# Performance work log

Measured on AMD Instinct MI355X. Metric: run time of the kernel, lower is better.

Reference implementation:

```python
import jax, jax.numpy as jnp
import numpy as np

HEAD = 16
CONV = 32
DEF = CONV * 8  # 256
SCALE = jnp.float32(np.sqrt(DEF))  # sqrt(256) = 16


def setup_inputs() -> dict:
    key = jax.random.key(0)
    k1, k2, k3, k4 = jax.random.split(key, 4)
    bsz = 4096
    drug = jax.random.normal(k1, (bsz, DEF), dtype=jnp.float32)
    protein = jax.random.normal(k2, (bsz, DEF), dtype=jnp.float32)
    # Linear(256 -> 4096) weights, stored [in, out]; bias zeros
    W_d = jax.random.normal(k3, (DEF, DEF * HEAD), dtype=jnp.float32) * (1.0 / np.sqrt(DEF))
    b_d = jnp.zeros((DEF * HEAD,), dtype=jnp.float32)
    W_p = jax.random.normal(k4, (DEF, DEF * HEAD), dtype=jnp.float32) * (1.0 / np.sqrt(DEF))
    b_p = jnp.zeros((DEF * HEAD,), dtype=jnp.float32)
    return {"drug": drug, "protein": protein, "W_d": W_d, "b_d": b_d, "W_p": W_p, "b_p": b_p}


def reference(drug, protein, W_d, b_d, W_p, b_p):
    bsz = drug.shape[0]
    # ReLU(linear) then reshape: drug -> [b, 256, head]; protein -> [b, head, 256]
    drug_att = jax.nn.relu(drug @ W_d + b_d).reshape(bsz, DEF, HEAD)
    protein_att = jax.nn.relu(protein @ W_p + b_p).reshape(bsz, HEAD, DEF)
    # interaction map [b, 256, 256]
    imap = jnp.tanh(jnp.einsum('bdh,bhp->bdp', drug_att, protein_att) / SCALE)
    compound_atte = jnp.tanh(jnp.sum(imap, axis=2))  # [b, 256]
    protein_atte = jnp.tanh(jnp.sum(imap, axis=1))   # [b, 256]
    return (drug * compound_atte, protein * protein_atte)
```

## Files before the change

kernel.cpp:

```cpp
#include <hip/hip_runtime.h>
#include <stdint.h>

typedef unsigned short u16;
typedef u16   u16x4 __attribute__((ext_vector_type(4)));
typedef u16   u16x8 __attribute__((ext_vector_type(8)));
typedef short v8s   __attribute__((ext_vector_type(8)));
typedef float v4f   __attribute__((ext_vector_type(4)));
typedef float f4    __attribute__((ext_vector_type(4)));

#if __has_builtin(__builtin_amdgcn_exp2f)
#define EXP2F(x) __builtin_amdgcn_exp2f(x)
#else
#define EXP2F(x) exp2f(x)
#endif
#if __has_builtin(__builtin_amdgcn_rcpf)
#define RCPF(x) __builtin_amdgcn_rcpf(x)
#else
#define RCPF(x) (1.0f/(x))
#endif

__device__ __forceinline__ float b2f(u16 u) {
    unsigned int i = ((unsigned int)u) << 16;
    float f; __builtin_memcpy(&f, &i, 4); return f;
}
__device__ __forceinline__ u16 f2b(float f) {
    unsigned int x; __builtin_memcpy(&x, &f, 4);
    x += 0x7fffu + ((x >> 16) & 1u);
    return (u16)(x >> 16);
}
__device__ __forceinline__ float tanhp(float x) {
    float e = EXP2F(2.8853900817779268f * x);
    return 1.0f - 2.0f * RCPF(1.0f + e);
}
__device__ __forceinline__ void g2l16(const u16* g, u16* l) {
    __builtin_amdgcn_global_load_lds(
        (const __attribute__((address_space(1))) unsigned int*)g,
        (__attribute__((address_space(3))) unsigned int*)l, 16, 0, 0);
}

#define RSCALE 0.42466090f

__global__ __launch_bounds__(256) void cvt_rows(
    const float* __restrict__ X0, const float* __restrict__ X1,
    u16* __restrict__ O0, u16* __restrict__ O1) {
    const float* X = blockIdx.z ? X1 : X0;
    u16*         O = blockIdx.z ? O1 : O0;
    size_t i = ((size_t)blockIdx.x * 256 + threadIdx.x) * 8;
    f4 a = *(const f4*)(X + i), b = *(const f4*)(X + i + 4);
    u16x8 r;
    r[0] = f2b(a[0]); r[1] = f2b(a[1]); r[2] = f2b(a[2]); r[3] = f2b(a[3]);
    r[4] = f2b(b[0]); r[5] = f2b(b[1]); r[6] = f2b(b[2]); r[7] = f2b(b[3]);
    *(u16x8*)(O + i) = r;
}

__global__ __launch_bounds__(256) void wtrans(
    const float* __restrict__ W0, const float* __restrict__ W1,
    u16* __restrict__ T0, u16* __restrict__ T1) {
    int z = blockIdx.z;
    const float* W = z ? W1 : W0;
    u16*         T = z ? T1 : T0;
    __shared__ u16 t[32][36];
    int k0 = blockIdx.x * 32, n0 = blockIdx.y * 32;
    int r = threadIdx.x >> 3, c = (threadIdx.x & 7) * 4;
    f4 v = *(const f4*)(W + (size_t)(k0 + r) * 4096 + n0 + c);
    t[r][c + 0] = f2b(v[0]); t[r][c + 1] = f2b(v[1]);
    t[r][c + 2] = f2b(v[2]); t[r][c + 3] = f2b(v[3]);
    __syncthreads();
    u16x4 o;
    o.x = t[c + 0][r]; o.y = t[c + 1][r]; o.z = t[c + 2][r]; o.w = t[c + 3][r];
    int n = n0 + r;
    int row = z ? ((n & 255) * 16 + (n >> 8)) : n;
    *(u16x4*)(T + (size_t)row * 256 + k0 + c) = o;
}

__global__ __launch_bounds__(256) void gemm_relu(
    const u16* __restrict__ A0, const u16* __restrict__ A1,
    const u16* __restrict__ B0, const u16* __restrict__ B1,
    const float* __restrict__ bias0, const float* __restrict__ bias1,
    u16* __restrict__ R0, u16* __restrict__ R1) {
    int z = blockIdx.z;
    const u16*   A    = z ? A1 : A0;
    const u16*   Bt   = z ? B1 : B0;
    const float* bias = z ? bias1 : bias0;
    u16*         R    = z ? R1 : R0;

    __shared__ __align__(16) u16 As[128 * 64];
    __shared__ __align__(16) u16 Bs[128 * 64];

    int tid  = threadIdx.x;
    int lane = tid & 63;
    int wave = tid >> 6;
    int m0 = blockIdx.x * 128, n0 = blockIdx.y * 128;
    int wm = (wave >> 1) * 64, wn = (wave & 1) * 64;

    v4f acc[4][4] = {};

    const u16* Ab = A  + (size_t)m0 * 256;
    const u16* Bb = Bt + (size_t)n0 * 256;
    int rsel = lane & 15, kg = lane >> 4;

    for (int kk = 0; kk < 256; kk += 64) {
        __syncthreads();
#pragma unroll
        for (int j = 0; j < 4; ++j) {
            int f = tid + j * 256;
            int r = f >> 3, cc = f & 7;
            int gc = (cc ^ (r & 7)) * 8;
            g2l16(Ab + (size_t)r * 256 + kk + gc, As + f * 8);
            g2l16(Bb + (size_t)r * 256 + kk + gc, Bs + f * 8);
        }
        __syncthreads();
#pragma unroll
        for (int h = 0; h < 2; ++h) {
            v8s af[4], bf[4];
#pragma unroll
            for (int mi = 0; mi < 4; mi++) {
                int row = wm + mi * 16 + rsel;
                af[mi] = *(const v8s*)(As + row * 64 + (((h * 4 + kg) ^ (row & 7)) * 8));
            }
#pragma unroll
            for (int ni = 0; ni < 4; ni++) {
                int row = wn + ni * 16 + rsel;
                bf[ni] = *(const v8s*)(Bs + row * 64 + (((h * 4 + kg) ^ (row & 7)) * 8));
            }
#pragma unroll
            for (int mi = 0; mi < 4; mi++)
#pragma unroll
                for (int ni = 0; ni < 4; ni++)
                    acc[mi][ni] = __builtin_amdgcn_mfma_f32_16x16x32_bf16(bf[ni], af[mi], acc[mi][ni], 0, 0, 0);
        }
    }

#pragma unroll
    for (int ni = 0; ni < 4; ni++) {
        int nb = n0 + wn + ni * 16 + kg * 4;
        float bv[4];
        if (z == 0) {
            f4 b4 = *(const f4*)(bias + nb);
#pragma unroll
            for (int t = 0; t < 4; ++t) bv[t] = b4[t];
        } else {
#pragma unroll
            for (int t = 0; t < 4; ++t) {
                int nn = nb + t;
                bv[t] = bias[(nn & 15) * 256 + (nn >> 4)];
            }
        }
#pragma unroll
        for (int mi = 0; mi < 4; mi++) {
            int m = m0 + wm + mi * 16 + rsel;
            u16x4 pack;
#pragma unroll
            for (int t = 0; t < 4; ++t)
                pack[t] = f2b(fmaxf(acc[mi][ni][t] + bv[t], 0.0f) * RSCALE);
            *(u16x4*)(R + (size_t)m * 4096 + nb) = pack;
        }
    }
}

__global__ __launch_bounds__(256, 4) void stage2(
    const u16* __restrict__ Rd, const u16* __restrict__ Rp,
    const float* __restrict__ drug, const float* __restrict__ protein,
    float* __restrict__ out, int bo) {
    int bl = blockIdx.x;
    int b  = bo + bl;
    __shared__ __align__(16) u16 Ad[4096];
    __shared__ __align__(16) u16 Bp[4096];
    float* rowq = (float*)Ad;
    float* colq = rowq + 256;

    int tid = threadIdx.x, lane = tid & 63, wave = tid >> 6;
    {
        const u16* rd = Rd + (size_t)bl * 4096;
        const u16* rp = Rp + (size_t)bl * 4096;
        g2l16(rd + tid * 8,         Ad + tid * 8);
        g2l16(rd + (tid + 256) * 8, Ad + (tid + 256) * 8);
        g2l16(rp + tid * 8,         Bp + tid * 8);
        g2l16(rp + (tid + 256) * 8, Bp + (tid + 256) * 8);
    }
    __syncthreads();

    int  mr = lane & 15;
    int  kg = lane >> 4;
    int  ko = (kg & 1) * 8;
    bool act = kg < 2;
    v8s zero8 = {};
    v4f czero = {};

    v8s af[4];
#pragma unroll
    for (int s = 0; s < 4; ++s) {
        v8s ld = *(const v8s*)(Ad + (wave * 64 + s * 16 + mr) * 16 + ko);
        af[s] = act ? ld : zero8;
    }
    __syncthreads();

    v4f rsq[4] = {czero, czero, czero, czero};
#pragma unroll 2
    for (int ni = 0; ni < 16; ++ni) {
        v8s bf = *(const v8s*)(Bp + (ni * 16 + mr) * 16 + ko);
        v4f cq = czero;
#pragma unroll
        for (int s = 0; s < 4; ++s) {
            v4f c = __builtin_amdgcn_mfma_f32_16x16x32_bf16(af[s], bf, czero, 0, 0, 0);
            v4f q;
#pragma unroll
            for (int t = 0; t < 4; ++t)
                q[t] = RCPF(1.0f + EXP2F(c[t]));
            rsq[s] += q;
            cq += q;
        }
        float cp = (cq[0] + cq[1]) + (cq[2] + cq[3]);
        cp += __shfl_xor(cp, 16);
        cp += __shfl_xor(cp, 32);
        if (lane < 16) colq[wave * 256 + ni * 16 + lane] = cp;
    }
#pragma unroll
    for (int s = 0; s < 4; ++s)
#pragma unroll
        for (int t = 0; t < 4; ++t) {
            float v = rsq[s][t];
            v += __shfl_xor(v, 1);
            v += __shfl_xor(v, 2);
            v += __shfl_xor(v, 4);
            v += __shfl_xor(v, 8);
            if (mr == 0) rowq[wave * 64 + s * 16 + kg * 4 + t] = v;
        }
    __syncthreads();
    float qc = colq[tid] + colq[256 + tid] + colq[512 + tid] + colq[768 + tid];
    float ca = tanhp(256.0f - 2.0f * rowq[tid]);
    float pa = tanhp(256.0f - 2.0f * qc);
    size_t o = (size_t)b * 256 + tid;
    out[o]           = drug[o]    * ca;
    out[1048576 + o] = protein[o] * pa;
}

__global__ __launch_bounds__(256) void fused_fallback(
    const float* __restrict__ drug, const float* __restrict__ protein,
    const float* __restrict__ Wd,   const float* __restrict__ bd,
    const float* __restrict__ Wp,   const float* __restrict__ bp,
    float* __restrict__ out)
{
    __shared__ __align__(16) u16 smem[73856];
    u16*   dRow = smem;
    u16*   pRow = smem + 2048;
    u16*   Ws   = smem + 4096;
    float* rowsum  = (float*)(smem + 4096);
    float* colpart = rowsum + 256;
    u16*   dAtt = smem + 8320;
    u16*   pAtt = smem + 41088;

    int tid = threadIdx.x, lane = tid & 63, wave = tid >> 6;
    int b0  = blockIdx.x * 8;
    int mr  = lane & 15;
    int kg  = lane >> 4;
    int ksel = kg * 8;

    {
        int row = tid >> 5, c = (tid & 31) * 8;
        const float* ps = drug + (size_t)(b0 + row) * 256 + c;
        const float* qs = protein + (size_t)(b0 + row) * 256 + c;
        u16x8 r1, r2;
#pragma unroll
        for (int j = 0; j < 8; ++j) { r1[j] = f2b(ps[j]); r2[j] = f2b(qs[j]); }
        *(u16x8*)(dRow + row * 256 + c) = r1;
        *(u16x8*)(pRow + row * 256 + c) = r2;
    }

    int r0 = tid >> 4;
    int c0 = (tid & 15) * 8;
    for (int which = 0; which < 2; ++which) {
        const float* W      = which ? Wp   : Wd;
        const float* bias   = which ? bp   : bd;
        const u16*   rowbuf = which ? pRow : dRow;
        u16*         att    = which ? pAtt : dAtt;

        for (int n0 = 0; n0 < 4096; n0 += 128) {
            v4f acc0 = {}, acc1 = {};
            int wn = wave * 32;
            u16x8 pf0, pf1;
            {
                const float* p0 = W + (size_t)(r0) * 4096 + n0 + c0;
                const float* p1 = W + (size_t)(r0 + 16) * 4096 + n0 + c0;
#pragma unroll
                for (int j = 0; j < 8; ++j) { pf0[j] = f2b(p0[j]); pf1[j] = f2b(p1[j]); }
            }
            for (int k0 = 0; k0 < 256; k0 += 32) {
                __syncthreads();
                *(u16x4*)(Ws + r0 * 132 + c0)            = ((u16x4*)&pf0)[0];
                *(u16x4*)(Ws + r0 * 132 + c0 + 4)        = ((u16x4*)&pf0)[1];
                *(u16x4*)(Ws + (r0 + 16) * 132 + c0)     = ((u16x4*)&pf1)[0];
                *(u16x4*)(Ws + (r0 + 16) * 132 + c0 + 4) = ((u16x4*)&pf1)[1];
                __syncthreads();
                if (k0 + 32 < 256) {
                    const float* p0 = W + (size_t)(k0 + 32 + r0) * 4096 + n0 + c0;
                    const float* p1 = W + (size_t)(k0 + 32 + r0 + 16) * 4096 + n0 + c0;
#pragma unroll
                    for (int j = 0; j < 8; ++j) { pf0[j] = f2b(p0[j]); pf1[j] = f2b(p1[j]); }
                }
                v8s af = {};
                if (mr < 8) af = *(const v8s*)(rowbuf + mr * 256 + k0 + ksel);
                v8s bf0, bf1;
                int nA = wn + mr, nB = wn + 16 + mr;
#pragma unroll
                for (int j = 0; j < 8; ++j) {
                    bf0[j] = (short)Ws[(ksel + j) * 132 + nA];
                    bf1[j] = (short)Ws[(ksel + j) * 132 + nB];
                }
                acc0 = __builtin_amdgcn_mfma_f32_16x16x32_bf16(af, bf0, acc0, 0, 0, 0);
                acc1 = __builtin_amdgcn_mfma_f32_16x16x32_bf16(af, bf1, acc1, 0, 0, 0);
            }
            int colA = n0 + wn + mr, colB = colA + 16;
            float bvA = bias[colA], bvB = bias[colB];
#pragma unroll
            for (int t = 0; t < 4; ++t) {
                int row = kg * 4 + t;
                if (row < 8) {
                    u16 vA = f2b(fmaxf(acc0[t] + bvA, 0.0f));
                    u16 vB = f2b(fmaxf(acc1[t] + bvB, 0.0f));
                    if (which == 0) {
                        att[row * 4096 + colA] = vA;
                        att[row * 4096 + colB] = vB;
                    } else {
                        att[row * 4096 + (colA & 255) * 16 + (colA >> 8)] = vA;
                        att[row * 4096 + (colB & 255) * 16 + (colB >> 8)] = vB;
                    }
                }
            }
        }
    }
    __syncthreads();

    v8s zero8 = {};
    v4f czero = {};
    int  ko2  = (kg & 1) * 8;
    bool act2 = kg < 2;
    for (int r = 0; r < 8; ++r) {
        const u16* Ar = dAtt + r * 4096;
        const u16* Br = pAtt + r * 4096;
        v8s af2[4];
#pragma unroll
        for (int s = 0; s < 4; ++s) {
            int d = wave * 64 + s * 16 + mr;
            v8s ld = *(const v8s*)(Ar + d * 16 + ko2);
            af2[s] = act2 ? ld : zero8;
        }
        float rs[4][4] = {};
#pragma unroll
        for (int ni = 0; ni < 16; ++ni) {
            int p = ni * 16 + mr;
            v8s lb = *(const v8s*)(Br + p * 16 + ko2);
            v8s bf = act2 ? lb : zero8;
            float cp = 0.0f;
#pragma unroll
            for (int s = 0; s < 4; ++s) {
                v4f c = __builtin_amdgcn_mfma_f32_16x16x32_bf16(af2[s], bf, czero, 0, 0, 0);
#pragma unroll
                for (int t = 0; t < 4; ++t) {
                    float v = tanhp(c[t] * 0.0625f);
                    rs[s][t] += v;
                    cp += v;
                }
            }
            cp += __shfl_xor(cp, 16);
            cp += __shfl_xor(cp, 32);
            if (lane < 16) colpart[wave * 256 + ni * 16 + lane] = cp;
        }
#pragma unroll
        for (int s = 0; s < 4; ++s)
#pragma unroll
            for (int t = 0; t < 4; ++t) {
                float v = rs[s][t];
                v += __shfl_xor(v, 1);
                v += __shfl_xor(v, 2);
                v += __shfl_xor(v, 4);
                v += __shfl_xor(v, 8);
                if (mr == 0) rowsum[wave * 64 + s * 16 + kg * 4 + t] = v;
            }
        __syncthreads();
        float cs = colpart[tid] + colpart[256 + tid] + colpart[512 + tid] + colpart[768 + tid];
        float ca = tanhp(rowsum[tid]);
        float pa = tanhp(cs);
        size_t o = (size_t)(b0 + r) * 256 + tid;
        out[o]           = drug[o]    * ca;
        out[1048576 + o] = protein[o] * pa;
        __syncthreads();
    }
}

extern "C" void kernel_launch(void* const* d_in, const int* in_sizes, int n_in,
                              void* d_out, int out_size, void* d_ws, size_t ws_size,
                              hipStream_t stream) {
    (void)in_sizes; (void)n_in; (void)out_size;
    const float* drug    = (const float*)d_in[0];
    const float* protein = (const float*)d_in[1];
    const float* Wd      = (const float*)d_in[2];
    const float* bd      = (const float*)d_in[3];
    const float* Wp      = (const float*)d_in[4];
    const float* bp      = (const float*)d_in[5];
    float* out = (float*)d_out;

    const size_t FIXED = (size_t)8 * 1024 * 1024;
    size_t avail = (ws_size > FIXED) ? ws_size - FIXED : 0;
    int chunk = (int)(avail / (2 * 4096 * sizeof(u16)));
    chunk = (chunk / 128) * 128;
    if (chunk > 4096) chunk = 4096;

    if (chunk >= 128) {
        u16* ws  = (u16*)d_ws;
        u16* Ad  = ws;
        u16* Ap  = Ad + (1u << 20);
        u16* Wtd = Ap + (1u << 20);
        u16* Wtp = Wtd + (1u << 20);
        u16* Rd  = Wtp + (1u << 20);
        u16* Rp  = Rd + (size_t)chunk * 4096;

        cvt_rows<<<dim3(512, 1, 2), 256, 0, stream>>>(drug, protein, Ad, Ap);
        wtrans  <<<dim3(8, 128, 2), 256, 0, stream>>>(Wd, Wp, Wtd, Wtp);
        for (int bo = 0; bo < 4096; bo += chunk) {
            int rows = (4096 - bo < chunk) ? (4096 - bo) : chunk;
            gemm_relu<<<dim3(rows / 128, 32, 2), 256, 0, stream>>>(
                Ad + (size_t)bo * 256, Ap + (size_t)bo * 256,
                Wtd, Wtp, bd, bp, Rd, Rp);
            stage2<<<dim3(rows), 256, 0, stream>>>(Rd, Rp, drug, protein, out, bo);
        }
    } else {
        fused_fallback<<<dim3(512), 256, 0, stream>>>(drug, protein, Wd, bd, Wp, bp, out);
    }
}
```

Baseline: 174.3 us.

## Merge prep kernels, enlarge GEMM tile to 256 rows, raise stage2 occupancy

The separate row-conversion and weight-transpose kernels become a single prep launch, which removes one kernel launch. The GEMM block grows to 512 threads and 256x128 tiles, so each B tile loaded into LDS is reused across twice as many rows. The stage2 launch bound is raised to 6 blocks per CU to ask for more occupancy, and chunking is now aligned to 256 rows. The trade-offs are more register pressure under the tighter bounds and fewer GEMM blocks to fill the GPU.

Result: no change. 175.1 us (+0.5%).

```diff
diff --git a/kernel.cpp b/kernel.cpp
--- a/kernel.cpp
+++ b/kernel.cpp
@@ -40,40 +40,40 @@
 
 #define RSCALE 0.42466090f
 
-__global__ __launch_bounds__(256) void cvt_rows(
-    const float* __restrict__ X0, const float* __restrict__ X1,
-    u16* __restrict__ O0, u16* __restrict__ O1) {
-    const float* X = blockIdx.z ? X1 : X0;
-    u16*         O = blockIdx.z ? O1 : O0;
-    size_t i = ((size_t)blockIdx.x * 256 + threadIdx.x) * 8;
-    f4 a = *(const f4*)(X + i), b = *(const f4*)(X + i + 4);
-    u16x8 r;
-    r[0] = f2b(a[0]); r[1] = f2b(a[1]); r[2] = f2b(a[2]); r[3] = f2b(a[3]);
-    r[4] = f2b(b[0]); r[5] = f2b(b[1]); r[6] = f2b(b[2]); r[7] = f2b(b[3]);
-    *(u16x8*)(O + i) = r;
-}
-
-__global__ __launch_bounds__(256) void wtrans(
-    const float* __restrict__ W0, const float* __restrict__ W1,
-    u16* __restrict__ T0, u16* __restrict__ T1) {
+__global__ __launch_bounds__(256) void prep(
+    const float* __restrict__ drug, const float* __restrict__ protein,
+    const float* __restrict__ Wd,   const float* __restrict__ Wp,
+    u16* __restrict__ Ad, u16* __restrict__ Ap,
+    u16* __restrict__ Wtd, u16* __restrict__ Wtp) {
     int z = blockIdx.z;
-    const float* W = z ? W1 : W0;
-    u16*         T = z ? T1 : T0;
-    __shared__ u16 t[32][36];
-    int k0 = blockIdx.x * 32, n0 = blockIdx.y * 32;
-    int r = threadIdx.x >> 3, c = (threadIdx.x & 7) * 4;
-    f4 v = *(const f4*)(W + (size_t)(k0 + r) * 4096 + n0 + c);
-    t[r][c + 0] = f2b(v[0]); t[r][c + 1] = f2b(v[1]);
-    t[r][c + 2] = f2b(v[2]); t[r][c + 3] = f2b(v[3]);
-    __syncthreads();
-    u16x4 o;
-    o.x = t[c + 0][r]; o.y = t[c + 1][r]; o.z = t[c + 2][r]; o.w = t[c + 3][r];
-    int n = n0 + r;
-    int row = z ? ((n & 255) * 16 + (n >> 8)) : n;
-    *(u16x4*)(T + (size_t)row * 256 + k0 + c) = o;
-}
-
-__global__ __launch_bounds__(256) void gemm_relu(
+    if (z < 2) {
+        const float* X = z ? protein : drug;
+        u16*         O = z ? Ap : Ad;
+        size_t i = ((size_t)blockIdx.x * 256 + threadIdx.x) * 4;
+        f4 a = *(const f4*)(X + i);
+        u16x4 r;
+        r[0] = f2b(a[0]); r[1] = f2b(a[1]); r[2] = f2b(a[2]); r[3] = f2b(a[3]);
+        *(u16x4*)(O + i) = r;
+    } else {
+        int zz = (z == 3);
+        const float* W = zz ? Wp : Wd;
+        u16*         T = zz ? Wtp : Wtd;
+        __shared__ u16 t[32][36];
+        int k0 = (blockIdx.x & 7) * 32, n0 = (blockIdx.x >> 3) * 32;
+        int r = threadIdx.x >> 3, c = (threadIdx.x & 7) * 4;
+        f4 v = *(const f4*)(W + (size_t)(k0 + r) * 4096 + n0 + c);
+        t[r][c + 0] = f2b(v[0]); t[r][c + 1] = f2b(v[1]);
+        t[r][c + 2] = f2b(v[2]); t[r][c + 3] = f2b(v[3]);
+        __syncthreads();
+        u16x4 o;
+        o.x = t[c + 0][r]; o.y = t[c + 1][r]; o.z = t[c + 2][r]; o.w = t[c + 3][r];
+        int n = n0 + r;
+        int row = zz ? ((n & 255) * 16 + (n >> 8)) : n;
+        *(u16x4*)(T + (size_t)row * 256 + k0 + c) = o;
+    }
+}
+
+__global__ __launch_bounds__(512, 4) void gemm_relu(
     const u16* __restrict__ A0, const u16* __restrict__ A1,
     const u16* __restrict__ B0, const u16* __restrict__ B1,
     const float* __restrict__ bias0, const float* __restrict__ bias1,
@@ -84,13 +84,13 @@
     const float* bias = z ? bias1 : bias0;
     u16*         R    = z ? R1 : R0;
 
-    __shared__ __align__(16) u16 As[128 * 64];
+    __shared__ __align__(16) u16 As[256 * 64];
     __shared__ __align__(16) u16 Bs[128 * 64];
 
     int tid  = threadIdx.x;
     int lane = tid & 63;
     int wave = tid >> 6;
-    int m0 = blockIdx.x * 128, n0 = blockIdx.y * 128;
+    int m0 = blockIdx.x * 256, n0 = blockIdx.y * 128;
     int wm = (wave >> 1) * 64, wn = (wave & 1) * 64;
 
     v4f acc[4][4] = {};
@@ -103,10 +103,16 @@
         __syncthreads();
 #pragma unroll
         for (int j = 0; j < 4; ++j) {
-            int f = tid + j * 256;
+            int f = tid + j * 512;
             int r = f >> 3, cc = f & 7;
             int gc = (cc ^ (r & 7)) * 8;
             g2l16(Ab + (size_t)r * 256 + kk + gc, As + f * 8);
+        }
+#pragma unroll
+        for (int j = 0; j < 2; ++j) {
+            int f = tid + j * 512;
+            int r = f >> 3, cc = f & 7;
+            int gc = (cc ^ (r & 7)) * 8;
             g2l16(Bb + (size_t)r * 256 + kk + gc, Bs + f * 8);
         }
         __syncthreads();
@@ -158,7 +164,7 @@
     }
 }
 
-__global__ __launch_bounds__(256, 4) void stage2(
+__global__ __launch_bounds__(256, 6) void stage2(
     const u16* __restrict__ Rd, const u16* __restrict__ Rp,
     const float* __restrict__ drug, const float* __restrict__ protein,
     float* __restrict__ out, int bo) {
@@ -403,10 +409,10 @@
     const size_t FIXED = (size_t)8 * 1024 * 1024;
     size_t avail = (ws_size > FIXED) ? ws_size - FIXED : 0;
     int chunk = (int)(avail / (2 * 4096 * sizeof(u16)));
-    chunk = (chunk / 128) * 128;
+    chunk = (chunk / 256) * 256;
     if (chunk > 4096) chunk = 4096;
 
-    if (chunk >= 128) {
+    if (chunk >= 256) {
         u16* ws  = (u16*)d_ws;
         u16* Ad  = ws;
         u16* Ap  = Ad + (1u << 20);
@@ -415,11 +421,10 @@
         u16* Rd  = Wtp + (1u << 20);
         u16* Rp  = Rd + (size_t)chunk * 4096;
 
-        cvt_rows<<<dim3(512, 1, 2), 256, 0, stream>>>(drug, protein, Ad, Ap);
-        wtrans  <<<dim3(8, 128, 2), 256, 0, stream>>>(Wd, Wp, Wtd, Wtp);
+        prep<<<dim3(1024, 1, 4), 256, 0, stream>>>(drug, protein, Wd, Wp, Ad, Ap, Wtd, Wtp);
         for (int bo = 0; bo < 4096; bo += chunk) {
             int rows = (4096 - bo < chunk) ? (4096 - bo) : chunk;
-            gemm_relu<<<dim3(rows / 128, 32, 2), 256, 0, stream>>>(
+            gemm_relu<<<dim3(rows / 256, 32, 2), 512, 0, stream>>>(
                 Ad + (size_t)bo * 256, Ap + (size_t)bo * 256,
                 Wtd, Wtp, bd, bp, Rd, Rp);
             stage2<<<dim3(rows), 256, 0, stream>>>(Rd, Rp, drug, protein, out, bo);
```
